# Kernel optimization log

Measured on AMD Instinct MI355X. Metric: run time of the kernel, lower is better.

The kernel has to match this reference:

```python
import jax, jax.numpy as jnp
import numpy as np

T, B, F = 197, 64, 768      # tokens (hardcoded 197 in module), batch, width
N, K = 8, 2                 # num_experts, top-k
CAP = int(197 * 1.0 * K / N)  # capacity = 49
H = 4 * F                   # expert hidden (c_fc out)
G = F // 4                  # gate hidden


def setup_inputs() -> dict:
    key = jax.random.key(0)
    ks = jax.random.split(key, 9)
    s = 0.02
    return {
        "x":   jax.random.normal(ks[0], (T, B, F), jnp.float32),
        # gate: Linear(F, F/4) -> ReLU -> Linear(F/4, N)
        "Wg1": jax.random.normal(ks[1], (F, G), jnp.float32) * s,
        "bg1": jnp.zeros((G,), jnp.float32),
        "Wg2": jax.random.normal(ks[2], (G, N), jnp.float32) * s,
        "bg2": jnp.zeros((N,), jnp.float32),
        # experts: per-expert Linear(F, 4F) -> ReLU -> Linear(4F, F), stacked over N
        "W1":  jax.random.normal(ks[3], (N, F, H), jnp.float32) * s,
        "b1":  jnp.zeros((N, H), jnp.float32),
        "W2":  jax.random.normal(ks[4], (N, H, F), jnp.float32) * s,
        "b2":  jnp.zeros((N, F), jnp.float32),
    }


def reference(x, Wg1, bg1, Wg2, bg2, W1, b1, W2, b2):
    # gating: softmax over experts (dim=2)
    logits = jax.nn.relu(x @ Wg1 + bg1) @ Wg2 + bg2          # [T,B,N]
    gw = jax.nn.softmax(logits, axis=2)                      # [T,B,N]

    # dense all-expert MLP (as-written: every expert on every token)
    h = jax.nn.relu(jnp.einsum('tbf,nfh->tbnh', x, W1) + b1)  # [T,B,N,H]
    eo = jnp.einsum('tbnh,nhf->tbnf', h, W2) + b2             # [T,B,N,F]

    # top-k expert mask (dim=2)
    _, idx = jax.lax.top_k(gw, K)                             # [T,B,K]
    mask_exp = jnp.any(jnp.arange(N)[None, None, None, :] == idx[..., None], axis=2)
    cw = gw * mask_exp                                        # [T,B,N]

    # capacity mask: top-CAP tokens per (batch, expert) along dim 0
    cwT = jnp.moveaxis(cw, 0, -1)                             # [B,N,T]
    _, idx2 = jax.lax.top_k(cwT, CAP)                         # [B,N,CAP]
    mask_cap = jnp.any(jnp.arange(T)[None, None, None, :] == idx2[..., None], axis=2)  # [B,N,T]
    fw = cw * jnp.moveaxis(mask_cap, -1, 0)                   # [T,B,N]

    # combine selected expert outputs, residual-style subtract
    out = jnp.einsum('tbnf,tbn->tbf', eo, fw) - x             # [T,B,F]
    return out
```

## Files before the change

kernel.cpp:

```cpp
#include <hip/hip_runtime.h>
#include <hip/hip_bf16.h>
#include <math.h>
#include <stdint.h>

#define T_ 197
#define B_ 64
#define F_ 768
#define N_ 8
#define CAP_ 49
#define H_ 3072
#define G_ 192
#define TB_ (T_*B_)
#define NBN_ (B_*N_)
#define ME_ 3200
#define MR_ 3136
#define MT_ 25600
#define KH_ 4
#define HCF_ 384
#define NPF_ 8

using bf16x8 = __attribute__((ext_vector_type(8))) short;
using f32x4  = __attribute__((ext_vector_type(4))) float;

__device__ __forceinline__ unsigned short f2bf(float v) {
    __hip_bfloat16 h = __float2bfloat16(v);
    return __builtin_bit_cast(unsigned short, h);
}
__device__ __forceinline__ float bf2f(unsigned short u) {
    unsigned int w = ((unsigned int)u) << 16;
    return __builtin_bit_cast(float, w);
}

#define GLL16(g, l) __builtin_amdgcn_global_load_lds( \
    (const __attribute__((address_space(1))) unsigned int*)(uintptr_t)(g), \
    (__attribute__((address_space(3))) unsigned int*)(uintptr_t)(l), 16, 0, 0)

__device__ __forceinline__ int xcd_swz(int bid, int nblk) {
    int q = nblk >> 3, r = nblk & 7;
    int xcd = bid & 7, idx = bid >> 3;
    int base = (xcd < r) ? xcd * (q + 1) : r * (q + 1) + (xcd - r) * q;
    return base + idx;
}

__global__ void k_init_out(const float* __restrict__ x, float* __restrict__ out) {
    int i = blockIdx.x * blockDim.x + threadIdx.x;
    const float4* xv = (const float4*)x;
    float4* ov = (float4*)out;
    float4 v = xv[i];
    ov[i] = make_float4(-v.x, -v.y, -v.z, -v.w);
}

__global__ __launch_bounds__(256) void k_gate1(
        const float* __restrict__ x, const float* __restrict__ Wg1,
        float* __restrict__ gs_part) {
    __shared__ float xs[32][68];
    __shared__ float wt[32][200];
    int bm = blockIdx.x % 197, kh = blockIdx.x / 197;
    int m0 = bm * 64, k0 = kh * (F_ / KH_);
    int tid = threadIdx.x, lane = tid & 63, wid = tid >> 6;
    int mg = lane & 15;
    int ng = (lane >> 4) + 4 * wid;
    f32x4 acc[4][3] = {};

    int xr = tid >> 3, xc = tid & 7;
    float4 xreg0, xreg1;
    float4 wreg[6];

    auto loadRegs = [&](int t) {
        int kb = k0 + t * 32;
        xreg0 = *(const float4*)(x + (size_t)(m0 + xr) * F_ + kb + xc * 4);
        xreg1 = *(const float4*)(x + (size_t)(m0 + xr + 32) * F_ + kb + xc * 4);
        #pragma unroll
        for (int i = 0; i < 6; ++i) {
            int idx = tid + i * 256;
            int kr = idx / 48, nc = idx % 48;
            wreg[i] = *(const float4*)(Wg1 + (size_t)(kb + kr) * G_ + nc * 4);
        }
    };
    auto writeLDS = [&]() {
        xs[xc * 4 + 0][xr] = xreg0.x;  xs[xc * 4 + 1][xr] = xreg0.y;
        xs[xc * 4 + 2][xr] = xreg0.z;  xs[xc * 4 + 3][xr] = xreg0.w;
        xs[xc * 4 + 0][xr + 32] = xreg1.x;  xs[xc * 4 + 1][xr + 32] = xreg1.y;
        xs[xc * 4 + 2][xr + 32] = xreg1.z;  xs[xc * 4 + 3][xr + 32] = xreg1.w;
        #pragma unroll
        for (int i = 0; i < 6; ++i) {
            int idx = tid + i * 256;
            int kr = idx / 48, nc = idx % 48;
            *(float4*)&wt[kr][nc * 4] = wreg[i];
        }
    };

    loadRegs(0);
    for (int t = 0; t < 6; ++t) {
        __syncthreads();
        writeLDS();
        __syncthreads();
        if (t < 5) loadRegs(t + 1);
        #pragma unroll
        for (int k = 0; k < 32; ++k) {
            float4 av = *(const float4*)&xs[k][mg * 4];
            float4 b0 = *(const float4*)&wt[k][ng * 12];
            float4 b1 = *(const float4*)&wt[k][ng * 12 + 4];
            float4 b2 = *(const float4*)&wt[k][ng * 12 + 8];
            float am[4] = {av.x, av.y, av.z, av.w};
            #pragma unroll
            for (int mi = 0; mi < 4; ++mi) {
                acc[mi][0][0] += am[mi] * b0.x; acc[mi][0][1] += am[mi] * b0.y;
                acc[mi][0][2] += am[mi] * b0.z; acc[mi][0][3] += am[mi] * b0.w;
                acc[mi][1][0] += am[mi] * b1.x; acc[mi][1][1] += am[mi] * b1.y;
                acc[mi][1][2] += am[mi] * b1.z; acc[mi][1][3] += am[mi] * b1.w;
                acc[mi][2][0] += am[mi] * b2.x; acc[mi][2][1] += am[mi] * b2.y;
                acc[mi][2][2] += am[mi] * b2.z; acc[mi][2][3] += am[mi] * b2.w;
            }
        }
    }
    float* gp = gs_part + (size_t)kh * TB_ * G_;
    #pragma unroll
    for (int mi = 0; mi < 4; ++mi) {
        int r = m0 + mg * 4 + mi;
        #pragma unroll
        for (int jv = 0; jv < 3; ++jv)
            *(f32x4*)(gp + (size_t)r * G_ + ng * 12 + jv * 4) = acc[mi][jv];
    }
}

__global__ __launch_bounds__(256) void k_gate2(
        const float* __restrict__ gs_part, const float* __restrict__ bg1,
        const float* __restrict__ Wg2, const float* __restrict__ bg2,
        float* __restrict__ cw, int* __restrict__ ecnt) {
    __shared__ float gsh[32][200];
    __shared__ float wg2s[G_ * N_];
    __shared__ float lg[32][8];
    int tid = threadIdx.x;
    int id0 = blockIdx.x * 32;

    for (int i = tid; i < 32 * 48; i += 256) {
        int r = i / 48, c4 = i % 48;
        const float* p0 = gs_part + (size_t)(id0 + r) * G_ + c4 * 4;
        float4 a = *(const float4*)p0;
        float4 b = *(const float4*)(p0 + (size_t)TB_ * G_);
        float4 c = *(const float4*)(p0 + 2 * (size_t)TB_ * G_);
        float4 d = *(const float4*)(p0 + 3 * (size_t)TB_ * G_);
        float4 g = *(const float4*)(bg1 + c4 * 4);
        float4 v;
        v.x = fmaxf(a.x + b.x + c.x + d.x + g.x, 0.f);
        v.y = fmaxf(a.y + b.y + c.y + d.y + g.y, 0.f);
        v.z = fmaxf(a.z + b.z + c.z + d.z + g.z, 0.f);
        v.w = fmaxf(a.w + b.w + c.w + d.w + g.w, 0.f);
        ((float4*)&gsh[r][0])[c4] = v;
    }
    for (int i = tid; i < G_ * N_; i += 256) wg2s[i] = Wg2[i];
    __syncthreads();

    int tk = tid >> 3, n = tid & 7;
    float a = bg2[n];
    for (int k = 0; k < G_; ++k) a += gsh[tk][k] * wg2s[k * N_ + n];
    lg[tk][n] = a;
    __syncthreads();

    if (tid < 32) {
        int tk2 = tid;
        float p[8];
        float m = lg[tk2][0];
        #pragma unroll
        for (int nn = 1; nn < 8; ++nn) m = fmaxf(m, lg[tk2][nn]);
        float s = 0.f;
        #pragma unroll
        for (int nn = 0; nn < 8; ++nn) { p[nn] = expf(lg[tk2][nn] - m); s += p[nn]; }
        float inv = 1.f / s;
        #pragma unroll
        for (int nn = 0; nn < 8; ++nn) p[nn] *= inv;
        int i1 = 0; float v1 = p[0];
        #pragma unroll
        for (int nn = 1; nn < 8; ++nn) if (p[nn] > v1) { v1 = p[nn]; i1 = nn; }
        int i2 = -1; float v2 = -1.f;
        #pragma unroll
        for (int nn = 0; nn < 8; ++nn) if (nn != i1 && p[nn] > v2) { v2 = p[nn]; i2 = nn; }
        int id = id0 + tk2;
        int t = id / B_, b = id % B_;
        ecnt[id] = 0;
        #pragma unroll
        for (int nn = 0; nn < 8; ++nn) {
            float v = (nn == i1 || nn == i2) ? p[nn] : 0.f;
            cw[((size_t)(b * N_ + nn)) * T_ + t] = v;
        }
    }
}

__global__ __launch_bounds__(256) void k_gate(
        const float* __restrict__ x, const float* __restrict__ Wg1,
        const float* __restrict__ bg1, const float* __restrict__ Wg2,
        const float* __restrict__ bg2, float* __restrict__ cw,
        int* __restrict__ ecnt) {
    __shared__ float xsh[8][F_];
    __shared__ float gsl[8][G_];
    __shared__ float lg[8][N_];
    int tid = threadIdx.x;
    int id0 = blockIdx.x * 8;

    int gid = blockIdx.x * 256 + tid;
    if (gid < TB_ && ecnt) ecnt[gid] = 0;

    const float4* xv = (const float4*)(x + (size_t)id0 * F_);
    float4* xshv = (float4*)&xsh[0][0];
    for (int idx = tid; idx < 8 * (F_/4); idx += 256) xshv[idx] = xv[idx];
    __syncthreads();

    if (tid < G_) {
        float acc[8];
        float bb = bg1[tid];
        #pragma unroll
        for (int tk = 0; tk < 8; ++tk) acc[tk] = bb;
        for (int k = 0; k < F_; ++k) {
            float w = Wg1[k * G_ + tid];
            #pragma unroll
            for (int tk = 0; tk < 8; ++tk) acc[tk] += xsh[tk][k] * w;
        }
        #pragma unroll
        for (int tk = 0; tk < 8; ++tk) gsl[tk][tid] = fmaxf(acc[tk], 0.f);
    }
    __syncthreads();

    if (tid < 64) {
        int tk = tid >> 3, n = tid & 7;
        float acc = bg2[n];
        for (int k = 0; k < G_; ++k) acc += gsl[tk][k] * Wg2[k * N_ + n];
        lg[tk][n] = acc;
    }
    __syncthreads();

    if (tid < 8) {
        int tk = tid;
        float p[8];
        float m = lg[tk][0];
        #pragma unroll
        for (int n = 1; n < 8; ++n) m = fmaxf(m, lg[tk][n]);
        float s = 0.f;
        #pragma unroll
        for (int n = 0; n < 8; ++n) { p[n] = expf(lg[tk][n] - m); s += p[n]; }
        float inv = 1.f / s;
        #pragma unroll
        for (int n = 0; n < 8; ++n) p[n] *= inv;
        int i1 = 0; float v1 = p[0];
        #pragma unroll
        for (int n = 1; n < 8; ++n) if (p[n] > v1) { v1 = p[n]; i1 = n; }
        int i2 = -1; float v2 = -1.f;
        #pragma unroll
        for (int n = 0; n < 8; ++n) if (n != i1 && p[n] > v2) { v2 = p[n]; i2 = n; }
        int id = id0 + tk;
        int t = id / B_, b = id % B_;
        #pragma unroll
        for (int n = 0; n < 8; ++n) {
            float v = (n == i1 || n == i2) ? p[n] : 0.f;
            cw[((size_t)(b * N_ + n)) * T_ + t] = v;
        }
    }
}

__global__ __launch_bounds__(256) void k_capacity(
        const float* __restrict__ cw, int* __restrict__ toks,
        float* __restrict__ wts, int* __restrict__ counts,
        int* __restrict__ ecnt, int* __restrict__ erow) {
    __shared__ float v[T_];
    __shared__ int keep[T_];
    int tid = threadIdx.x;
    int bn = blockIdx.x;
    int b = bn >> 3, n = bn & 7;
    if (tid < T_) v[tid] = cw[(size_t)bn * T_ + tid];
    __syncthreads();
    int kp = 0; float my = 0.f;
    if (tid < T_) {
        my = v[tid];
        int rank = 0;
        for (int t2 = 0; t2 < T_; ++t2) {
            float vt = v[t2];
            rank += (vt > my) || (vt == my && t2 < tid);
        }
        kp = (rank < CAP_) && (my > 0.f);
    }
    if (tid < T_) keep[tid] = kp;
    __syncthreads();
    if (tid < T_ && kp) {
        int slot = 0;
        for (int t2 = 0; t2 < T_; ++t2) slot += (t2 < tid) ? keep[t2] : 0;
        toks[bn * CAP_ + slot] = tid;
        wts[bn * CAP_ + slot] = my;
        if (ecnt) {
            int orow = tid * B_ + b;
            int pos = atomicAdd(&ecnt[orow], 1);
            erow[orow * 2 + pos] = n * ME_ + b * CAP_ + slot;
        }
    }
    if (tid == 0) {
        int tot = 0;
        for (int t2 = 0; t2 < T_; ++t2) tot += keep[t2];
        counts[bn] = tot;
    }
}

__global__ __launch_bounds__(256) void k_repack(
        const float* __restrict__ W, unsigned short* __restrict__ WT, int K, int J) {
    __shared__ float tile[64][65];
    int bid = blockIdx.x;
    int nk = K >> 6, nj = J >> 6;
    int kt = bid % nk; bid /= nk;
    int jt = bid % nj; int e = bid / nj;
    int k0 = kt * 64, j0 = jt * 64;
    int tid = threadIdx.x;
    int jr = (tid & 15) << 2;
    int kr = tid >> 4;
    const float* src = W + ((size_t)e * K + k0) * J + j0;
    #pragma unroll
    for (int i = 0; i < 4; ++i) {
        float4 v = *(const float4*)(src + (size_t)(kr + 16 * i) * J + jr);
        *(float4*)&tile[kr + 16 * i][jr] = v;
    }
    __syncthreads();
    int c = tid & 7;
    int jrow = tid >> 3;
    #pragma unroll
    for (int i = 0; i < 2; ++i) {
        int j = jrow + 32 * i;
        float f[8];
        #pragma unroll
        for (int s = 0; s < 8; ++s) f[s] = tile[c * 8 + s][j];
        uint4 u;
        u.x = f2bf(f[0]) | ((unsigned)f2bf(f[1]) << 16);
        u.y = f2bf(f[2]) | ((unsigned)f2bf(f[3]) << 16);
        u.z = f2bf(f[4]) | ((unsigned)f2bf(f[5]) << 16);
        u.w = f2bf(f[6]) | ((unsigned)f2bf(f[7]) << 16);
        int jg = j0 + j;
        char* drow = (char*)WT + ((size_t)e * J + jg) * (size_t)K * 2 + (size_t)(k0 >> 6) * 128;
        *(uint4*)(drow + ((c << 4) ^ ((jg & 7) << 4))) = u;
    }
}

__global__ __launch_bounds__(256) void k_gather(
        const float* __restrict__ x, const int* __restrict__ toks,
        const int* __restrict__ counts, unsigned short* __restrict__ Xg) {
    int gi = blockIdx.x * 256 + threadIdx.x;
    int R = gi / 96, c = gi - R * 96;
    int e = R / ME_, re = R - e * ME_;
    uint4 val = make_uint4(0u, 0u, 0u, 0u);
    if (re < MR_) {
        int g = re / CAP_, slot = re - g * CAP_;
        int bn = g * N_ + e;
        if (slot < counts[bn]) {
            int t = toks[bn * CAP_ + slot];
            const float* xp = x + ((size_t)t * B_ + g) * F_ + c * 8;
            float4 v0 = *(const float4*)xp;
            float4 v1 = *(const float4*)(xp + 4);
            val.x = f2bf(v0.x) | ((unsigned)f2bf(v0.y) << 16);
            val.y = f2bf(v0.z) | ((unsigned)f2bf(v0.w) << 16);
            val.z = f2bf(v1.x) | ((unsigned)f2bf(v1.y) << 16);
            val.w = f2bf(v1.z) | ((unsigned)f2bf(v1.w) << 16);
        }
    }
    int w = (c * 16) & 127;
    char* dst = (char*)Xg + (size_t)R * 1536 + (c >> 3) * 128 + (w ^ ((R & 7) << 4));
    *(uint4*)dst = val;
}

__global__ __launch_bounds__(256) void k_gemm1(
        const unsigned short* __restrict__ W1T, const unsigned short* __restrict__ Xg,
        const float* __restrict__ b1, unsigned short* __restrict__ Hg,
        int e0, int nblk) {
    __shared__ char ldsA[2][16384];
    __shared__ char ldsB[2][16384];
    int swzb = xcd_swz(blockIdx.x, nblk);
    int mt = swzb / 24;
    int jt = swzb % 24;
    int em = mt / 25;
    int e = e0 + em;
    int tid = threadIdx.x, lane = tid & 63, wid = tid >> 6;
    int lr8 = lane >> 3, sl = (lane & 7) << 4;
    const char* Ab = (const char*)W1T + ((size_t)e * H_ + (size_t)jt * 128) * (F_ * 2);
    const char* Bb = (const char*)Xg + ((size_t)e * ME_ + (size_t)(mt % 25) * 128) * (F_ * 2);
    f32x4 acc[4][4] = {};
    int swz = (lane & 7) << 4;
    int q16 = (lane >> 4) << 4;

    auto stage = [&](int buf, int it) {
        int kb = it << 7;
        #pragma unroll
        for (int i = 0; i < 4; ++i) {
            int lr = wid * 32 + i * 8 + lr8;
            GLL16(Ab + (size_t)lr * 1536 + kb + sl, ldsA[buf] + (wid * 32 + i * 8) * 128);
            GLL16(Bb + (size_t)lr * 1536 + kb + sl, ldsB[buf] + (wid * 32 + i * 8) * 128);
        }
    };

    stage(0, 0);
    __syncthreads();
    int cur = 0;
    for (int it = 0; it < 12; ++it) {
        if (it < 11) stage(cur ^ 1, it + 1);
        const char* la = ldsA[cur] + ((wid & 1) * 64) * 128;
        const char* lb = ldsB[cur] + ((wid >> 1) * 64) * 128;
        #pragma unroll
        for (int ks = 0; ks < 2; ++ks) {
            bf16x8 af[4], bfr[4];
            int kk = (ks * 64 + q16) ^ swz;
            #pragma unroll
            for (int t = 0; t < 4; ++t) {
                int ro = (16 * t + (lane & 15)) * 128;
                af[t]  = *(const bf16x8*)(la + ro + kk);
                bfr[t] = *(const bf16x8*)(lb + ro + kk);
            }
            #pragma unroll
            for (int ti = 0; ti < 4; ++ti)
                #pragma unroll
                for (int tm = 0; tm < 4; ++tm)
                    acc[ti][tm] = __builtin_amdgcn_mfma_f32_16x16x32_bf16(af[ti], bfr[tm], acc[ti][tm], 0, 0, 0);
        }
        __syncthreads();
        cur ^= 1;
    }
    char* tile = &ldsA[0][0];
    int jl0 = (wid & 1) * 64;
    int ml0 = (wid >> 1) * 64;
    const float* b1p = b1 + (size_t)e * H_ + (size_t)jt * 128;
    #pragma unroll
    for (int tj = 0; tj < 4; ++tj) {
        int jc = jl0 + 16 * tj + ((lane >> 4) << 2);
        float bb0 = b1p[jc], bb1 = b1p[jc + 1], bb2 = b1p[jc + 2], bb3 = b1p[jc + 3];
        #pragma unroll
        for (int tm = 0; tm < 4; ++tm) {
            int m = ml0 + 16 * tm + (lane & 15);
            f32x4 a = acc[tj][tm];
            unsigned int u0 = f2bf(fmaxf(a[0] + bb0, 0.f)) | ((unsigned)f2bf(fmaxf(a[1] + bb1, 0.f)) << 16);
            unsigned int u1 = f2bf(fmaxf(a[2] + bb2, 0.f)) | ((unsigned)f2bf(fmaxf(a[3] + bb3, 0.f)) << 16);
            int bcol = jc * 2;
            int w = bcol & 127;
            *(uint2*)(tile + m * 256 + (bcol & ~127) + (w ^ ((m & 7) << 4))) = make_uint2(u0, u1);
        }
    }
    __syncthreads();
    char* Hrow = (char*)Hg + (size_t)(mt * 128) * (H_ * 2) + (size_t)jt * 256;
    #pragma unroll
    for (int i = 0; i < 8; ++i) {
        int idx = tid + i * 256;
        int r = idx >> 4, c = (idx & 15) << 4;
        *(uint4*)(Hrow + (size_t)r * (H_ * 2) + c) = *(const uint4*)(tile + r * 256 + c);
    }
}

__global__ __launch_bounds__(256) void k_gemm2(
        const unsigned short* __restrict__ W2T, const unsigned short* __restrict__ Hg,
        const float* __restrict__ b2, const float* __restrict__ wts,
        const int* __restrict__ counts, unsigned short* __restrict__ Og,
        int e0, int nblk) {
    __shared__ char ldsA[2][16384];
    __shared__ char ldsB[2][16384];
    int swzb = xcd_swz(blockIdx.x, nblk);
    int mt = swzb / 6;
    int ft = swzb % 6;
    int em = mt / 25;
    int e = e0 + em;
    int tid = threadIdx.x, lane = tid & 63, wid = tid >> 6;
    int lr8 = lane >> 3, sl = (lane & 7) << 4;
    const char* Ab = (const char*)W2T + ((size_t)e * F_ + (size_t)ft * 128) * (H_ * 2);
    const char* Bb = (const char*)Hg + (size_t)mt * 128 * (H_ * 2);
    f32x4 acc[4][4] = {};
    int swz = (lane & 7) << 4;
    int q16 = (lane >> 4) << 4;

    auto stage = [&](int buf, int it) {
        int kb = it << 7;
        #pragma unroll
        for (int i = 0; i < 4; ++i) {
            int lr = wid * 32 + i * 8 + lr8;
            GLL16(Ab + (size_t)lr * 6144 + kb + sl, ldsA[buf] + (wid * 32 + i * 8) * 128);
            GLL16(Bb + (size_t)lr * 6144 + kb + sl, ldsB[buf] + (wid * 32 + i * 8) * 128);
        }
    };

    stage(0, 0);
    __syncthreads();
    int cur = 0;
    for (int it = 0; it < 48; ++it) {
        if (it < 47) stage(cur ^ 1, it + 1);
        const char* la = ldsA[cur] + ((wid & 1) * 64) * 128;
        const char* lb = ldsB[cur] + ((wid >> 1) * 64) * 128;
        #pragma unroll
        for (int ks = 0; ks < 2; ++ks) {
            bf16x8 af[4], bfr[4];
            int kk = (ks * 64 + q16) ^ swz;
            #pragma unroll
            for (int t = 0; t < 4; ++t) {
                int ro = (16 * t + (lane & 15)) * 128;
                af[t]  = *(const bf16x8*)(la + ro + kk);
                bfr[t] = *(const bf16x8*)(lb + ro + kk);
            }
            #pragma unroll
            for (int ti = 0; ti < 4; ++ti)
                #pragma unroll
                for (int tm = 0; tm < 4; ++tm)
                    acc[ti][tm] = __builtin_amdgcn_mfma_f32_16x16x32_bf16(af[ti], bfr[tm], acc[ti][tm], 0, 0, 0);
        }
        __syncthreads();
        cur ^= 1;
    }
    char* tile = &ldsA[0][0];
    int fl0 = (wid & 1) * 64;
    int ml0 = (wid >> 1) * 64;
    const float* b2p = b2 + (size_t)e * F_ + (size_t)ft * 128;
    float fwv[4];
    #pragma unroll
    for (int tm = 0; tm < 4; ++tm) {
        int mloc = ml0 + 16 * tm + (lane & 15);
        int re = mt * 128 + mloc - em * ME_;
        float fw = 0.f;
        if (re < MR_) {
            int g = re / CAP_;
            int slot = re - g * CAP_;
            int bn = g * N_ + e;
            if (slot < counts[bn]) fw = wts[bn * CAP_ + slot];
        }
        fwv[tm] = fw;
    }
    #pragma unroll
    for (int tf = 0; tf < 4; ++tf) {
        int fc = fl0 + 16 * tf + ((lane >> 4) << 2);
        float c0 = b2p[fc], c1 = b2p[fc + 1], c2 = b2p[fc + 2], c3 = b2p[fc + 3];
        #pragma unroll
        for (int tm = 0; tm < 4; ++tm) {
            int mloc = ml0 + 16 * tm + (lane & 15);
            f32x4 a = acc[tf][tm];
            float fw = fwv[tm];
            unsigned int u0 = f2bf(fw * (a[0] + c0)) | ((unsigned)f2bf(fw * (a[1] + c1)) << 16);
            unsigned int u1 = f2bf(fw * (a[2] + c2)) | ((unsigned)f2bf(fw * (a[3] + c3)) << 16);
            int bcol = fc * 2;
            int w = bcol & 127;
            *(uint2*)(tile + mloc * 256 + (bcol & ~127) + (w ^ ((mloc & 7) << 4))) = make_uint2(u0, u1);
        }
    }
    __syncthreads();
    char* Orow = (char*)Og + ((size_t)(e0 * ME_ + mt * 128)) * (F_ * 2) + (size_t)ft * 256;
    #pragma unroll
    for (int i = 0; i < 8; ++i) {
        int idx = tid + i * 256;
        int r = idx >> 4, c = (idx & 15) << 4;
        const char* src = tile + r * 256 + (c & ~127) + ((c & 127) ^ ((r & 7) << 4));
        *(uint4*)(Orow + (size_t)r * (F_ * 2) + c) = *(const uint4*)src;
    }
}

__global__ __launch_bounds__(256) void k_combine(
        const float* __restrict__ x, const unsigned short* __restrict__ Og,
        const int* __restrict__ ecnt, const int* __restrict__ erow,
        float* __restrict__ out) {
    int idx = blockIdx.x * 256 + threadIdx.x;
    int row = idx / 192, c4 = idx - row * 192;
    float4 s = make_float4(0.f, 0.f, 0.f, 0.f);
    int c = ecnt[row];
    if (c > 0) {
        ushort4 u = *(const ushort4*)(Og + (size_t)erow[row * 2] * F_ + c4 * 4);
        s.x += bf2f(u.x); s.y += bf2f(u.y); s.z += bf2f(u.z); s.w += bf2f(u.w);
    }
    if (c > 1) {
        ushort4 u = *(const ushort4*)(Og + (size_t)erow[row * 2 + 1] * F_ + c4 * 4);
        s.x += bf2f(u.x); s.y += bf2f(u.y); s.z += bf2f(u.z); s.w += bf2f(u.w);
    }
    float4 xv = ((const float4*)x)[idx];
    ((float4*)out)[idx] = make_float4(s.x - xv.x, s.y - xv.y, s.z - xv.z, s.w - xv.w);
}

__global__ __launch_bounds__(HCF_) void k_fc1(
        const float* __restrict__ x, const float* __restrict__ W1,
        const float* __restrict__ b1, const int* __restrict__ toks,
        const int* __restrict__ counts, __hip_bfloat16* __restrict__ h, int pass) {
    __shared__ float xs[25][F_];
    int tid = threadIdx.x;
    int bn = blockIdx.x >> 1;
    int half = blockIdx.x & 1;
    int r0 = half * 25;
    int b = bn >> 3, n = bn & 7;
    int c = counts[bn];
    for (int idx = tid; idx < 25 * (F_/4); idx += HCF_) {
        int r = idx / (F_/4), k4 = idx % (F_/4);
        int gr = r0 + r;
        float4 val = make_float4(0.f, 0.f, 0.f, 0.f);
        if (gr < c) {
            int t = toks[bn * CAP_ + gr];
            val = ((const float4*)(x + ((size_t)(t * B_ + b)) * F_))[k4];
        }
        ((float4*)&xs[r][0])[k4] = val;
    }
    __syncthreads();
    int j = pass * HCF_ + tid;
    const float* w1p = W1 + (size_t)n * F_ * H_ + j;
    float bias = b1[n * H_ + j];
    float acc[25];
    #pragma unroll
    for (int r = 0; r < 25; ++r) acc[r] = bias;
    const float4* xsv = (const float4*)&xs[0][0];
    for (int k4 = 0; k4 < F_/4; ++k4) {
        float w0 = w1p[(size_t)(4*k4+0) * H_];
        float w1v = w1p[(size_t)(4*k4+1) * H_];
        float w2v = w1p[(size_t)(4*k4+2) * H_];
        float w3v = w1p[(size_t)(4*k4+3) * H_];
        #pragma unroll
        for (int r = 0; r < 25; ++r) {
            float4 xv = xsv[r * (F_/4) + k4];
            acc[r] += xv.x*w0 + xv.y*w1v + xv.z*w2v + xv.w*w3v;
        }
    }
    __hip_bfloat16* hp = h + ((size_t)bn * CAP_ + r0) * HCF_ + tid;
    #pragma unroll
    for (int r = 0; r < 25; ++r) {
        int gr = r0 + r;
        if (gr < CAP_) hp[(size_t)r * HCF_] = __float2bfloat16(fmaxf(acc[r], 0.f));
    }
}

__global__ __launch_bounds__(768) void k_fc2(
        const float* __restrict__ W2, const float* __restrict__ b2,
        const int* __restrict__ toks, const float* __restrict__ wts,
        const int* __restrict__ counts, const __hip_bfloat16* __restrict__ h,
        float* __restrict__ out, int pass) {
    __shared__ float hs[CAP_][HCF_];
    int tid = threadIdx.x;
    int bn = blockIdx.x;
    int c = counts[bn];
    if (c == 0) return;
    int b = bn >> 3, n = bn & 7;
    const ushort4* hv = (const ushort4*)(h + (size_t)bn * CAP_ * HCF_);
    for (int idx = tid; idx < CAP_ * (HCF_/4); idx += 768) {
        ushort4 u = hv[idx];
        float4 fv;
        fv.x = __bfloat162float(*(const __hip_bfloat16*)&u.x);
        fv.y = __bfloat162float(*(const __hip_bfloat16*)&u.y);
        fv.z = __bfloat162float(*(const __hip_bfloat16*)&u.z);
        fv.w = __bfloat162float(*(const __hip_bfloat16*)&u.w);
        ((float4*)&hs[0][0])[idx] = fv;
    }
    __syncthreads();
    int f = tid;
    const float* w2p = W2 + (size_t)n * H_ * F_ + (size_t)(pass * HCF_) * F_ + f;
    float acc[CAP_];
    #pragma unroll
    for (int r = 0; r < CAP_; ++r) acc[r] = 0.f;
    for (int j4 = 0; j4 < HCF_/4; ++j4) {
        float w0 = w2p[(size_t)(4*j4+0) * F_];
        float w1v = w2p[(size_t)(4*j4+1) * F_];
        float w2v = w2p[(size_t)(4*j4+2) * F_];
        float w3v = w2p[(size_t)(4*j4+3) * F_];
        #pragma unroll
        for (int r = 0; r < CAP_; ++r) {
            float4 hh = ((const float4*)&hs[r][0])[j4];
            acc[r] += hh.x*w0 + hh.y*w1v + hh.z*w2v + hh.w*w3v;
        }
    }
    float bias = (pass == 0) ? b2[n * F_ + f] : 0.f;
    #pragma unroll
    for (int r = 0; r < CAP_; ++r) {
        if (r < c) {
            int t = toks[bn * CAP_ + r];
            float fw = wts[bn * CAP_ + r];
            atomicAdd(&out[((size_t)(t * B_ + b)) * F_ + f], fw * (acc[r] + bias));
        }
    }
}

extern "C" void kernel_launch(void* const* d_in, const int* in_sizes, int n_in,
                              void* d_out, int out_size, void* d_ws, size_t ws_size,
                              hipStream_t stream) {
    const float* x   = (const float*)d_in[0];
    const float* Wg1 = (const float*)d_in[1];
    const float* bg1 = (const float*)d_in[2];
    const float* Wg2 = (const float*)d_in[3];
    const float* bg2 = (const float*)d_in[4];
    const float* W1  = (const float*)d_in[5];
    const float* b1  = (const float*)d_in[6];
    const float* W2  = (const float*)d_in[7];
    const float* b2  = (const float*)d_in[8];
    float* out = (float*)d_out;

    size_t oW1T  = 0;
    size_t oW2T  = oW1T + (size_t)N_ * H_ * F_ * 2;
    size_t oXg   = oW2T + (size_t)N_ * H_ * F_ * 2;
    size_t oCw   = oXg  + (size_t)MT_ * F_ * 2;
    size_t oWts  = oCw  + (size_t)NBN_ * T_ * 4;
    size_t oTok  = oWts + (size_t)NBN_ * CAP_ * 4;
    size_t oCnt  = oTok + (size_t)NBN_ * CAP_ * 4;
    size_t oEcnt = oCnt + (size_t)NBN_ * 4;
    size_t oErow = oEcnt + (size_t)TB_ * 4;
    size_t oOg   = oErow + (size_t)TB_ * 8;
    size_t oHg   = oOg  + (size_t)MT_ * F_ * 2;
    size_t hgPerExpert = (size_t)ME_ * H_ * 2;

    int grp = 0;
    if (ws_size >= oHg + 8 * hgPerExpert) grp = 8;
    else if (ws_size >= oHg + 4 * hgPerExpert) grp = 4;
    else if (ws_size >= oHg + 2 * hgPerExpert) grp = 2;

    if (grp > 0) {
        unsigned short* W1T = (unsigned short*)((char*)d_ws + oW1T);
        unsigned short* W2T = (unsigned short*)((char*)d_ws + oW2T);
        unsigned short* Xg  = (unsigned short*)((char*)d_ws + oXg);
        unsigned short* Og  = (unsigned short*)((char*)d_ws + oOg);
        unsigned short* Hg  = (unsigned short*)((char*)d_ws + oHg);
        float* gs_part = (float*)((char*)d_ws + oHg);
        float* cw   = (float*)((char*)d_ws + oCw);
        float* wts  = (float*)((char*)d_ws + oWts);
        int* toks   = (int*)((char*)d_ws + oTok);
        int* counts = (int*)((char*)d_ws + oCnt);
        int* ecnt   = (int*)((char*)d_ws + oEcnt);
        int* erow   = (int*)((char*)d_ws + oErow);

        k_gate1<<<197 * KH_, 256, 0, stream>>>(x, Wg1, gs_part);
        k_gate2<<<TB_ / 32, 256, 0, stream>>>(gs_part, bg1, Wg2, bg2, cw, ecnt);
        k_capacity<<<NBN_, 256, 0, stream>>>(cw, toks, wts, counts, ecnt, erow);
        k_repack<<<N_ * (F_/64) * (H_/64), 256, 0, stream>>>(W1, W1T, F_, H_);
        k_repack<<<N_ * (H_/64) * (F_/64), 256, 0, stream>>>(W2, W2T, H_, F_);
        k_gather<<<(MT_ * 96) / 256, 256, 0, stream>>>(x, toks, counts, Xg);
        for (int e0 = 0; e0 < N_; e0 += grp) {
            int nblk1 = grp * 25 * 24;
            int nblk2 = grp * 25 * 6;
            k_gemm1<<<nblk1, 256, 0, stream>>>(W1T, Xg, b1, Hg, e0, nblk1);
            k_gemm2<<<nblk2, 256, 0, stream>>>(W2T, Hg, b2, wts, counts, Og, e0, nblk2);
        }
        k_combine<<<(TB_ * 192) / 256, 256, 0, stream>>>(x, Og, ecnt, erow, out);
    } else {
        __hip_bfloat16* h = (__hip_bfloat16*)d_ws;
        float* cw  = (float*)((char*)d_ws + (size_t)NBN_ * CAP_ * HCF_ * 2);
        float* wts = cw + (size_t)NBN_ * T_;
        int* toks  = (int*)(wts + NBN_ * CAP_);
        int* counts = toks + NBN_ * CAP_;
        k_init_out<<<(TB_ * F_) / 1024, 256, 0, stream>>>(x, out);
        k_gate<<<TB_ / 8, 256, 0, stream>>>(x, Wg1, bg1, Wg2, bg2, cw, nullptr);
        k_capacity<<<NBN_, 256, 0, stream>>>(cw, toks, wts, counts, nullptr, nullptr);
        for (int p = 0; p < NPF_; ++p) {
            k_fc1<<<NBN_ * 2, HCF_, 0, stream>>>(x, W1, b1, toks, counts, h, p);
            k_fc2<<<NBN_, 768, 0, stream>>>(W2, b2, toks, wts, counts, h, out, p);
        }
    }
}
```

Before: 507.2 us.

## Split expert hidden dimension into four passes with accumulated bf16 partial outputs

Restructures the expert MLP so the hidden dimension is processed in four chunks of 768 across all experts at once. Each pass computes an H slice in gemm1 and a partial gemm2 that accumulates into the output buffer via read-add-write in bf16. The H intermediate shrinks to a quarter and gemm2 grids grow from 150/expert-group blocks to 1200 blocks, giving more parallelism and a smaller workspace footprint. In exchange the output gets extra read-modify-write traffic and repeated bf16 rounding of partial sums, which loses accuracy.

```diff
diff --git a/kernel.cpp b/kernel.cpp
--- a/kernel.cpp
+++ b/kernel.cpp
@@ -16,6 +16,8 @@
 #define MR_ 3136
 #define MT_ 25600
 #define KH_ 4
+#define HP_ 768
+#define NBLK_ 1200
 #define HCF_ 384
 #define NPF_ 8
 
@@ -29,6 +31,11 @@
 __device__ __forceinline__ float bf2f(unsigned short u) {
     unsigned int w = ((unsigned int)u) << 16;
     return __builtin_bit_cast(float, w);
+}
+__device__ __forceinline__ unsigned int add2bf(unsigned int a, unsigned int b) {
+    float al = bf2f((unsigned short)(a & 0xffff)), ah = bf2f((unsigned short)(a >> 16));
+    float bl = bf2f((unsigned short)(b & 0xffff)), bh = bf2f((unsigned short)(b >> 16));
+    return (unsigned int)f2bf(al + bl) | ((unsigned int)f2bf(ah + bh) << 16);
 }
 
 #define GLL16(g, l) __builtin_amdgcn_global_load_lds( \
@@ -363,19 +370,17 @@
 
 __global__ __launch_bounds__(256) void k_gemm1(
         const unsigned short* __restrict__ W1T, const unsigned short* __restrict__ Xg,
-        const float* __restrict__ b1, unsigned short* __restrict__ Hg,
-        int e0, int nblk) {
+        const float* __restrict__ b1, unsigned short* __restrict__ Hg, int pass) {
     __shared__ char ldsA[2][16384];
     __shared__ char ldsB[2][16384];
-    int swzb = xcd_swz(blockIdx.x, nblk);
-    int mt = swzb / 24;
-    int jt = swzb % 24;
-    int em = mt / 25;
-    int e = e0 + em;
+    int swzb = xcd_swz(blockIdx.x, NBLK_);
+    int e = swzb / 150;
+    int rem = swzb - e * 150;
+    int mt = rem / 6, jt = rem % 6;
     int tid = threadIdx.x, lane = tid & 63, wid = tid >> 6;
     int lr8 = lane >> 3, sl = (lane & 7) << 4;
-    const char* Ab = (const char*)W1T + ((size_t)e * H_ + (size_t)jt * 128) * (F_ * 2);
-    const char* Bb = (const char*)Xg + ((size_t)e * ME_ + (size_t)(mt % 25) * 128) * (F_ * 2);
+    const char* Ab = (const char*)W1T + ((size_t)e * H_ + pass * HP_ + jt * 128) * (F_ * 2);
+    const char* Bb = (const char*)Xg + ((size_t)e * ME_ + mt * 128) * (F_ * 2);
     f32x4 acc[4][4] = {};
     int swz = (lane & 7) << 4;
     int q16 = (lane >> 4) << 4;
@@ -419,7 +424,7 @@
     char* tile = &ldsA[0][0];
     int jl0 = (wid & 1) * 64;
     int ml0 = (wid >> 1) * 64;
-    const float* b1p = b1 + (size_t)e * H_ + (size_t)jt * 128;
+    const float* b1p = b1 + (size_t)e * H_ + pass * HP_ + jt * 128;
     #pragma unroll
     for (int tj = 0; tj < 4; ++tj) {
         int jc = jl0 + 16 * tj + ((lane >> 4) << 2);
@@ -436,31 +441,29 @@
         }
     }
     __syncthreads();
-    char* Hrow = (char*)Hg + (size_t)(mt * 128) * (H_ * 2) + (size_t)jt * 256;
+    char* Hrow = (char*)Hg + ((size_t)e * ME_ + mt * 128) * (HP_ * 2) + (size_t)jt * 256;
     #pragma unroll
     for (int i = 0; i < 8; ++i) {
         int idx = tid + i * 256;
         int r = idx >> 4, c = (idx & 15) << 4;
-        *(uint4*)(Hrow + (size_t)r * (H_ * 2) + c) = *(const uint4*)(tile + r * 256 + c);
+        *(uint4*)(Hrow + (size_t)r * (HP_ * 2) + c) = *(const uint4*)(tile + r * 256 + c);
     }
 }
 
 __global__ __launch_bounds__(256) void k_gemm2(
         const unsigned short* __restrict__ W2T, const unsigned short* __restrict__ Hg,
         const float* __restrict__ b2, const float* __restrict__ wts,
-        const int* __restrict__ counts, unsigned short* __restrict__ Og,
-        int e0, int nblk) {
+        const int* __restrict__ counts, unsigned short* __restrict__ Og, int pass) {
     __shared__ char ldsA[2][16384];
     __shared__ char ldsB[2][16384];
-    int swzb = xcd_swz(blockIdx.x, nblk);
-    int mt = swzb / 6;
-    int ft = swzb % 6;
-    int em = mt / 25;
-    int e = e0 + em;
+    int swzb = xcd_swz(blockIdx.x, NBLK_);
+    int e = swzb / 150;
+    int rem = swzb - e * 150;
+    int mt = rem / 6, ft = rem % 6;
     int tid = threadIdx.x, lane = tid & 63, wid = tid >> 6;
     int lr8 = lane >> 3, sl = (lane & 7) << 4;
-    const char* Ab = (const char*)W2T + ((size_t)e * F_ + (size_t)ft * 128) * (H_ * 2);
-    const char* Bb = (const char*)Hg + (size_t)mt * 128 * (H_ * 2);
+    const char* Ab = (const char*)W2T + ((size_t)e * F_ + ft * 128) * (H_ * 2) + (size_t)pass * (HP_ * 2);
+    const char* Bb = (const char*)Hg + ((size_t)e * ME_ + mt * 128) * (HP_ * 2);
     f32x4 acc[4][4] = {};
     int swz = (lane & 7) << 4;
     int q16 = (lane >> 4) << 4;
@@ -471,15 +474,15 @@
         for (int i = 0; i < 4; ++i) {
             int lr = wid * 32 + i * 8 + lr8;
             GLL16(Ab + (size_t)lr * 6144 + kb + sl, ldsA[buf] + (wid * 32 + i * 8) * 128);
-            GLL16(Bb + (size_t)lr * 6144 + kb + sl, ldsB[buf] + (wid * 32 + i * 8) * 128);
+            GLL16(Bb + (size_t)lr * 1536 + kb + sl, ldsB[buf] + (wid * 32 + i * 8) * 128);
         }
     };
 
     stage(0, 0);
     __syncthreads();
     int cur = 0;
-    for (int it = 0; it < 48; ++it) {
-        if (it < 47) stage(cur ^ 1, it + 1);
+    for (int it = 0; it < 12; ++it) {
+        if (it < 11) stage(cur ^ 1, it + 1);
         const char* la = ldsA[cur] + ((wid & 1) * 64) * 128;
         const char* lb = ldsB[cur] + ((wid >> 1) * 64) * 128;
         #pragma unroll
@@ -509,7 +512,7 @@
     #pragma unroll
     for (int tm = 0; tm < 4; ++tm) {
         int mloc = ml0 + 16 * tm + (lane & 15);
-        int re = mt * 128 + mloc - em * ME_;
+        int re = mt * 128 + mloc;
         float fw = 0.f;
         if (re < MR_) {
             int g = re / CAP_;
@@ -522,7 +525,8 @@
     #pragma unroll
     for (int tf = 0; tf < 4; ++tf) {
         int fc = fl0 + 16 * tf + ((lane >> 4) << 2);
-        float c0 = b2p[fc], c1 = b2p[fc + 1], c2 = b2p[fc + 2], c3 = b2p[fc + 3];
+        float c0 = 0.f, c1 = 0.f, c2 = 0.f, c3 = 0.f;
+        if (pass == 0) { c0 = b2p[fc]; c1 = b2p[fc + 1]; c2 = b2p[fc + 2]; c3 = b2p[fc + 3]; }
         #pragma unroll
         for (int tm = 0; tm < 4; ++tm) {
             int mloc = ml0 + 16 * tm + (lane & 15);
@@ -536,13 +540,31 @@
         }
     }
     __syncthreads();
-    char* Orow = (char*)Og + ((size_t)(e0 * ME_ + mt * 128)) * (F_ * 2) + (size_t)ft * 256;
-    #pragma unroll
-    for (int i = 0; i < 8; ++i) {
-        int idx = tid + i * 256;
-        int r = idx >> 4, c = (idx & 15) << 4;
-        const char* src = tile + r * 256 + (c & ~127) + ((c & 127) ^ ((r & 7) << 4));
-        *(uint4*)(Orow + (size_t)r * (F_ * 2) + c) = *(const uint4*)src;
+    char* Orow = (char*)Og + ((size_t)e * ME_ + mt * 128) * (F_ * 2) + (size_t)ft * 256;
+    if (pass == 0) {
+        #pragma unroll
+        for (int i = 0; i < 8; ++i) {
+            int idx = tid + i * 256;
+            int r = idx >> 4, c = (idx & 15) << 4;
+            const char* src = tile + r * 256 + (c & ~127) + ((c & 127) ^ ((r & 7) << 4));
+            *(uint4*)(Orow + (size_t)r * (F_ * 2) + c) = *(const uint4*)src;
+        }
+    } else {
+        #pragma unroll
+        for (int i = 0; i < 8; ++i) {
+            int idx = tid + i * 256;
+            int r = idx >> 4, c = (idx & 15) << 4;
+            const char* src = tile + r * 256 + (c & ~127) + ((c & 127) ^ ((r & 7) << 4));
+            uint4 nw = *(const uint4*)src;
+            uint4* dst = (uint4*)(Orow + (size_t)r * (F_ * 2) + c);
+            uint4 old = *dst;
+            uint4 res;
+            res.x = add2bf(old.x, nw.x);
+            res.y = add2bf(old.y, nw.y);
+            res.z = add2bf(old.z, nw.z);
+            res.w = add2bf(old.w, nw.w);
+            *dst = res;
+        }
     }
 }
 
@@ -688,14 +710,9 @@
     size_t oErow = oEcnt + (size_t)TB_ * 4;
     size_t oOg   = oErow + (size_t)TB_ * 8;
     size_t oHg   = oOg  + (size_t)MT_ * F_ * 2;
-    size_t hgPerExpert = (size_t)ME_ * H_ * 2;
-
-    int grp = 0;
-    if (ws_size >= oHg + 8 * hgPerExpert) grp = 8;
-    else if (ws_size >= oHg + 4 * hgPerExpert) grp = 4;
-    else if (ws_size >= oHg + 2 * hgPerExpert) grp = 2;
-
-    if (grp > 0) {
+    size_t need  = oHg + (size_t)MT_ * HP_ * 2;
+
+    if (ws_size >= need) {
         unsigned short* W1T = (unsigned short*)((char*)d_ws + oW1T);
         unsigned short* W2T = (unsigned short*)((char*)d_ws + oW2T);
         unsigned short* Xg  = (unsigned short*)((char*)d_ws + oXg);
@@ -715,11 +732,9 @@
         k_repack<<<N_ * (F_/64) * (H_/64), 256, 0, stream>>>(W1, W1T, F_, H_);
         k_repack<<<N_ * (H_/64) * (F_/64), 256, 0, stream>>>(W2, W2T, H_, F_);
         k_gather<<<(MT_ * 96) / 256, 256, 0, stream>>>(x, toks, counts, Xg);
-        for (int e0 = 0; e0 < N_; e0 += grp) {
-            int nblk1 = grp * 25 * 24;
-            int nblk2 = grp * 25 * 6;
-            k_gemm1<<<nblk1, 256, 0, stream>>>(W1T, Xg, b1, Hg, e0, nblk1);
-            k_gemm2<<<nblk2, 256, 0, stream>>>(W2T, Hg, b2, wts, counts, Og, e0, nblk2);
+        for (int p = 0; p < 4; ++p) {
+            k_gemm1<<<NBLK_, 256, 0, stream>>>(W1T, Xg, b1, Hg, p);
+            k_gemm2<<<NBLK_, 256, 0, stream>>>(W2T, Hg, b2, wts, counts, Og, p);
         }
         k_combine<<<(TB_ * 192) / 256, 256, 0, stream>>>(x, Og, ecnt, erow, out);
     } else {
```

Result: no change. 507.0 us (-0.0%).
